# Optimization experiments

Measured on AMD Instinct MI355X. Metric: run time of the kernel, lower is better.

## Reference

```python
import jax, jax.numpy as jnp
import numpy as np

N_QUBITS = 12
DEPTH = 6
BATCH = 4096

# Wire 0 is the most-significant bit (PennyLane default.qubit convention).

def _rx(t):
    c = jnp.cos(t / 2).astype(jnp.complex64)
    s = (-1j * jnp.sin(t / 2)).astype(jnp.complex64)
    return jnp.stack([jnp.stack([c, s], -1), jnp.stack([s, c], -1)], -2)

def _ry(t):
    c = jnp.cos(t / 2).astype(jnp.complex64)
    s = jnp.sin(t / 2).astype(jnp.complex64)
    return jnp.stack([jnp.stack([c, -s], -1), jnp.stack([s, c], -1)], -2)

def _rz(t):
    em = jnp.exp(-1j * t.astype(jnp.complex64) / 2)
    ep = jnp.exp(1j * t.astype(jnp.complex64) / 2)
    z = jnp.zeros_like(em)
    return jnp.stack([jnp.stack([em, z], -1), jnp.stack([z, ep], -1)], -2)

def _apply_1q(state, gate, q, n):
    # state: (B, 2^n); gate: (2,2) shared or (B,2,2) batched
    B = state.shape[0]
    st = state.reshape(B, 1 << q, 2, 1 << (n - 1 - q))
    eq = 'ab,xlbr->xlar' if gate.ndim == 2 else 'xab,xlbr->xlar'
    return jnp.einsum(eq, gate, st).reshape(B, -1)

def _apply_cnot(state, c, n):
    # CNOT with control c, target c+1 (adjacent wires)
    B = state.shape[0]
    st = state.reshape(B, 1 << c, 2, 2, 1 << (n - 2 - c))
    st = jnp.concatenate([st[:, :, 0:1], st[:, :, 1:2, ::-1]], axis=2)
    return st.reshape(B, -1)

def _z_signs(n):
    idx = jnp.arange(1 << n)
    bits = (idx[None, :] >> (n - 1 - jnp.arange(n))[:, None]) & 1  # (n, 2^n)
    return (1.0 - 2.0 * bits).astype(jnp.float32)

def setup_inputs() -> dict:
    key = jax.random.key(0)
    k1, k2 = jax.random.split(key)
    x = jax.random.normal(k1, (BATCH, N_QUBITS), dtype=jnp.float32)
    params = jax.random.normal(k2, (DEPTH, N_QUBITS, 3), dtype=jnp.float32)
    return {"x": x, "params": params}

def reference(x, params):
    B, n = x.shape
    depth = params.shape[0]
    state = jnp.zeros((B, 1 << n), jnp.complex64).at[:, 0].set(1.0)
    # input encoding: batched RX per qubit
    for i in range(n):
        state = _apply_1q(state, _rx(x[:, i]), i, n)
    for d in range(depth):
        for i in range(n):
            state = _apply_1q(state, _ry(params[d, i, 0]), i, n)
            state = _apply_1q(state, _rz(params[d, i, 1]), i, n)
            state = _apply_1q(state, _rx(params[d, i, 2]), i, n)
        for i in range(n - 1):
            state = _apply_cnot(state, i, n)
    probs = state.real ** 2 + state.imag ** 2  # (B, 2^n)
    return probs @ _z_signs(n).T  # (B, n) Pauli-Z expvals
```

## Files before the change

### kernel.cpp

```cpp
#include <hip/hip_runtime.h>

#define NQ    12
#define DIM   4096
#define DEPTH 6
#define BLK   256
#define RJ    16


typedef float f32x2 __attribute__((ext_vector_type(2)));

__device__ __host__ __forceinline__ constexpr int sufxc(int v) {
  v ^= v >> 1; v ^= v >> 2; v ^= v >> 4; v ^= v >> 8; return v;
}
__device__ __host__ __forceinline__ constexpr int K1w(int j) { return (j << 4) ^ j; }
__device__ __host__ __forceinline__ constexpr int K2w(int j) { return j << 8; }
__device__ __host__ __forceinline__ constexpr int KCw(int j) {
  const int s4 = sufxc(j) & 15;
  const int p  = __builtin_popcount((unsigned)j) & 1;
  return (s4 << 8) | (p ? 0xF0 : 0);
}

__device__ __forceinline__ f32x2 pfma(f32x2 a, f32x2 b, f32x2 c) {
  return __builtin_elementwise_fma(a, b, c);
}

template <int B>
__device__ __forceinline__ void gate4(f32x2 (&amp)[RJ], float4 u0, float4 u1) {
  const f32x2 r00 = {u0.x, u0.x}, mi00 = {-u0.y, u0.y};
  const f32x2 r01 = {u0.z, u0.z}, mi01 = {-u0.w, u0.w};
  const f32x2 r10 = {u1.x, u1.x}, mi10 = {-u1.y, u1.y};
  const f32x2 r11 = {u1.z, u1.z}, mi11 = {-u1.w, u1.w};
#pragma unroll
  for (int m = 0; m < RJ / 2; ++m) {
    const int lo = m & ((1 << B) - 1);
    const int j0 = ((m >> B) << (B + 1)) | lo;
    const int j1 = j0 | (1 << B);
    const f32x2 a = amp[j0], b = amp[j1];
    const f32x2 ax = a.yx, bx = b.yx;
    f32x2 n0 = r00 * a;
    n0 = pfma(mi00, ax, n0);
    n0 = pfma(r01, b, n0);
    n0 = pfma(mi01, bx, n0);
    f32x2 n1 = r10 * a;
    n1 = pfma(mi10, ax, n1);
    n1 = pfma(r11, b, n1);
    n1 = pfma(mi11, bx, n1);
    amp[j0] = n0; amp[j1] = n1;
  }
}

__global__ void gate_prep(const float* __restrict__ params, float* __restrict__ gt) {
  const int T = threadIdx.x;
  if (T >= DEPTH * NQ) return;
  const float py = params[T * 3 + 0];
  const float pz = params[T * 3 + 1];
  const float px = params[T * 3 + 2];
  float sa, ca, sb, cb, sg, cg;
  __sincosf(py * 0.5f, &sa, &ca);
  __sincosf(pz * 0.5f, &sb, &cb);
  __sincosf(px * 0.5f, &sg, &cg);
  const float Ar = ca * cb, Ai = -ca * sb;
  const float Br = -sa * cb, Bi = sa * sb;
  const float Cr = sa * cb, Ci = sa * sb;
  const float Dr = ca * cb, Di = ca * sb;
  float* u = &gt[T * 8];
  u[0] = cg * Ar + sg * Ci;   u[1] = cg * Ai - sg * Cr;
  u[2] = cg * Br + sg * Di;   u[3] = cg * Bi - sg * Dr;
  u[4] = sg * Ai + cg * Cr;   u[5] = -sg * Ar + cg * Ci;
  u[6] = sg * Bi + cg * Dr;   u[7] = -sg * Br + cg * Di;
}

__global__ __launch_bounds__(BLK) void qsim_kernel(const float* __restrict__ x,
                                                   const float* __restrict__ gt,
                                                   float* __restrict__ out) {
  __shared__ f32x2 sm2[DIM];

  const int T = threadIdx.x;
  const int b = blockIdx.x;

  f32x2 amp[RJ];
  {
    float cs[NQ], sn[NQ];
#pragma unroll
    for (int i = 0; i < NQ; ++i) __sincosf(x[b * NQ + i] * 0.5f, &sn[i], &cs[i]);
    float hm = 1.0f;
#pragma unroll
    for (int i = 0; i < 8; ++i) hm *= ((T >> (7 - i)) & 1) ? sn[i] : cs[i];
    float mag[RJ];
    mag[0] = hm;
#pragma unroll
    for (int bb = 0; bb < 4; ++bb) {
#pragma unroll
      for (int j = 0; j < (1 << bb); ++j) {
        mag[j | (1 << bb)] = mag[j] * sn[11 - bb];
        mag[j] = mag[j] * cs[11 - bb];
      }
    }
    const int pt = __popc(T);
#pragma unroll
    for (int j = 0; j < RJ; ++j) {
      const float m = mag[j];
      const int k = (pt + __popc(j)) & 3;
      const float rr = (k & 1) ? 0.0f : ((k & 2) ? -m : m);
      const float ii = (k & 1) ? ((k & 2) ? m : -m) : 0.0f;
      amp[j] = (f32x2){rr, ii};
    }
  }

  const int A0w = (T << 4) ^ (T & 15);
  const int B0w = ((T >> 4) << 8) | (T & 15);
  const int C0w = T ^ ((T >> 4) & 15);
  const int CT  = sufxc(T) & 255;
  const int D0w = CT ^ ((CT >> 4) & 15);

#define SWEEP(D, WBASE)                                                       \
  {                                                                           \
    const float4* uv0 = (const float4*)&gt[((D) * NQ + (WBASE)) * 8];         \
    gate4<0>(amp, uv0[0], uv0[1]);                                            \
    const float4* uv1 = (const float4*)&gt[((D) * NQ + (WBASE) - 1) * 8];     \
    gate4<1>(amp, uv1[0], uv1[1]);                                            \
    const float4* uv2 = (const float4*)&gt[((D) * NQ + (WBASE) - 2) * 8];     \
    gate4<2>(amp, uv2[0], uv2[1]);                                            \
    const float4* uv3 = (const float4*)&gt[((D) * NQ + (WBASE) - 3) * 8];     \
    gate4<3>(amp, uv3[0], uv3[1]);                                            \
  }
#define ST_ALL(EXPR)                                                          \
  {                                                                           \
    _Pragma("unroll") for (int j = 0; j < RJ; ++j) { sm2[(EXPR)] = amp[j]; }  \
  }
#define LD_ALL(EXPR)                                                          \
  {                                                                           \
    _Pragma("unroll") for (int j = 0; j < RJ; ++j) { amp[j] = sm2[(EXPR)]; }  \
  }

#pragma unroll 1
  for (int d = 0; d < DEPTH; ++d) {
    SWEEP(d, 11)
    ST_ALL(A0w ^ j)
    LD_ALL(B0w ^ K1w(j))
    SWEEP(d, 7)
    ST_ALL(B0w ^ K1w(j))
    __syncthreads();
    LD_ALL(C0w ^ K2w(j))
    SWEEP(d, 3)
    __syncthreads();
    ST_ALL(D0w ^ KCw(j))
    __syncthreads();
    LD_ALL(A0w ^ j)
  }
#undef SWEEP
#undef ST_ALL
#undef LD_ALL

  float tot = 0.f, s0 = 0.f, s1 = 0.f, s2 = 0.f, s3 = 0.f;
#pragma unroll
  for (int j = 0; j < RJ; ++j) {
    const float p = fmaf(amp[j].x, amp[j].x, amp[j].y * amp[j].y);
    tot += p;
    s0 += (j & 1) ? -p : p;
    s1 += (j & 2) ? -p : p;
    s2 += (j & 4) ? -p : p;
    s3 += (j & 8) ? -p : p;
  }
  float v[NQ];
#pragma unroll
  for (int w = 0; w < 8; ++w) v[w] = ((T >> (7 - w)) & 1) ? -tot : tot;
  v[8] = s3; v[9] = s2; v[10] = s1; v[11] = s0;
#pragma unroll
  for (int w = 0; w < NQ; ++w) {
#pragma unroll
    for (int o = 32; o > 0; o >>= 1) v[w] += __shfl_xor(v[w], o);
  }
  __syncthreads();
  const int wv = T >> 6, lt = T & 63;
  float* smf = (float*)sm2;
  if (lt == 0) {
#pragma unroll
    for (int w = 0; w < NQ; ++w) smf[w * 4 + wv] = v[w];
  }
  __syncthreads();
  if (T < NQ) out[b * NQ + T] = (smf[T * 4 + 0] + smf[T * 4 + 1]) +
                                (smf[T * 4 + 2] + smf[T * 4 + 3]);
}

extern "C" void kernel_launch(void* const* d_in, const int* in_sizes, int n_in,
                              void* d_out, int out_size, void* d_ws, size_t ws_size,
                              hipStream_t stream) {
  const float* x      = (const float*)d_in[0];
  const float* params = (const float*)d_in[1];
  float* out          = (float*)d_out;
  float* gt           = (float*)d_ws;
  const int B = in_sizes[0] / NQ;
  gate_prep<<<1, 128, 0, stream>>>(params, gt);
  qsim_kernel<<<B, BLK, 0, stream>>>(x, gt, out);
}
```

Baseline: 238.2 us.

## Apply fused 4-qubit gate blocks via bf16 split-precision MFMA matrix multiplies

Replaces the per-thread scalar 2x2 gate sweeps with 16x16 complex unitaries, one per group of four wires, built by a prep kernel as Kronecker products. These are applied with bf16 MFMA instructions, using a hi/lo bf16 split of both the matrix and the state to keep near-fp32 accuracy. The state now lives in LDS as packed split-bf16 values with swizzled addressing, and the final probabilities are written to LDS for the reduction. The aim is to move the gate arithmetic onto the matrix cores, at the cost of extra pack/unpack work, more LDS traffic, more barriers, and some precision loss from the split representation.

```diff
diff --git a/kernel.cpp b/kernel.cpp
--- a/kernel.cpp
+++ b/kernel.cpp
@@ -4,81 +4,202 @@
 #define DIM   4096
 #define DEPTH 6
 #define BLK   256
-#define RJ    16
-
-
-typedef float f32x2 __attribute__((ext_vector_type(2)));
-
-__device__ __host__ __forceinline__ constexpr int sufxc(int v) {
-  v ^= v >> 1; v ^= v >> 2; v ^= v >> 4; v ^= v >> 8; return v;
-}
-__device__ __host__ __forceinline__ constexpr int K1w(int j) { return (j << 4) ^ j; }
-__device__ __host__ __forceinline__ constexpr int K2w(int j) { return j << 8; }
-__device__ __host__ __forceinline__ constexpr int KCw(int j) {
-  const int s4 = sufxc(j) & 15;
-  const int p  = __builtin_popcount((unsigned)j) & 1;
-  return (s4 << 8) | (p ? 0xF0 : 0);
-}
-
-__device__ __forceinline__ f32x2 pfma(f32x2 a, f32x2 b, f32x2 c) {
-  return __builtin_elementwise_fma(a, b, c);
-}
-
-template <int B>
-__device__ __forceinline__ void gate4(f32x2 (&amp)[RJ], float4 u0, float4 u1) {
-  const f32x2 r00 = {u0.x, u0.x}, mi00 = {-u0.y, u0.y};
-  const f32x2 r01 = {u0.z, u0.z}, mi01 = {-u0.w, u0.w};
-  const f32x2 r10 = {u1.x, u1.x}, mi10 = {-u1.y, u1.y};
-  const f32x2 r11 = {u1.z, u1.z}, mi11 = {-u1.w, u1.w};
-#pragma unroll
-  for (int m = 0; m < RJ / 2; ++m) {
-    const int lo = m & ((1 << B) - 1);
-    const int j0 = ((m >> B) << (B + 1)) | lo;
-    const int j1 = j0 | (1 << B);
-    const f32x2 a = amp[j0], b = amp[j1];
-    const f32x2 ax = a.yx, bx = b.yx;
-    f32x2 n0 = r00 * a;
-    n0 = pfma(mi00, ax, n0);
-    n0 = pfma(r01, b, n0);
-    n0 = pfma(mi01, bx, n0);
-    f32x2 n1 = r10 * a;
-    n1 = pfma(mi10, ax, n1);
-    n1 = pfma(r11, b, n1);
-    n1 = pfma(mi11, bx, n1);
-    amp[j0] = n0; amp[j1] = n1;
-  }
-}
-
-__global__ void gate_prep(const float* __restrict__ params, float* __restrict__ gt) {
-  const int T = threadIdx.x;
-  if (T >= DEPTH * NQ) return;
-  const float py = params[T * 3 + 0];
-  const float pz = params[T * 3 + 1];
-  const float px = params[T * 3 + 2];
-  float sa, ca, sb, cb, sg, cg;
-  __sincosf(py * 0.5f, &sa, &ca);
-  __sincosf(pz * 0.5f, &sb, &cb);
-  __sincosf(px * 0.5f, &sg, &cg);
-  const float Ar = ca * cb, Ai = -ca * sb;
-  const float Br = -sa * cb, Bi = sa * sb;
-  const float Cr = sa * cb, Ci = sa * sb;
-  const float Dr = ca * cb, Di = ca * sb;
-  float* u = &gt[T * 8];
-  u[0] = cg * Ar + sg * Ci;   u[1] = cg * Ai - sg * Cr;
-  u[2] = cg * Br + sg * Di;   u[3] = cg * Bi - sg * Dr;
-  u[4] = sg * Ai + cg * Cr;   u[5] = -sg * Ar + cg * Ci;
-  u[6] = sg * Bi + cg * Dr;   u[7] = -sg * Br + cg * Di;
+#define NT    4
+
+
+typedef __attribute__((ext_vector_type(8))) short bfrag;
+typedef __attribute__((ext_vector_type(4))) float f32x4v;
+typedef __attribute__((ext_vector_type(4))) int   i32x4v;
+typedef __attribute__((ext_vector_type(2))) unsigned u32x2v;
+
+__device__ __host__ __forceinline__ constexpr int sfx4(int v) {
+  v &= 15; v ^= v >> 1; v ^= v >> 2; return v & 15;
+}
+__device__ __host__ __forceinline__ constexpr int sfx8(int v) {
+  v &= 255; v ^= v >> 1; v ^= v >> 2; v ^= v >> 4; return v & 255;
+}
+__device__ __host__ __forceinline__ constexpr int par4(int v) {
+  return __builtin_popcount((unsigned)v) & 1;
+}
+__device__ __forceinline__ int pa(int c, int comp, int l) {
+  int uu = (comp << 2) | (l >> 2);
+  uu = (uu ^ (c & 7) ^ ((c >> 4) & 7)) & 7;
+  return (c << 7) + (uu << 4) + ((l & 3) << 2);
+}
+__device__ __host__ __forceinline__ constexpr int pa0(int cd, int ld) {
+  return (cd << 7) ^ (((((cd & 7) ^ ((cd >> 4) & 7)) ^ ((ld >> 2) & 3)) & 7) << 4)
+                   ^ ((ld & 3) << 2);
+}
+__device__ __host__ __forceinline__ constexpr int prodK(int P, int dd) {
+  return (P == 0) ? pa0(dd, 0)
+       : (P == 1) ? pa0(dd << 4, 0)
+       : pa0((sfx4(dd) << 4) | (par4(dd) * 15), par4(dd) * 15);
+}
+__device__ __host__ __forceinline__ constexpr int qK(int dd) {
+  return (sfx4(dd) << 8) | (par4(dd) * 255);
+}
+
+__device__ __forceinline__ unsigned rne16(unsigned u) {
+  return (u + 0x7FFFu + ((u >> 16) & 1u)) >> 16;
+}
+__device__ __forceinline__ unsigned packsplit(float x) {
+  const unsigned u = __float_as_uint(x);
+  const unsigned h = rne16(u);
+  const float hf = __uint_as_float(h << 16);
+  const unsigned l = rne16(__float_as_uint(x - hf));
+  return h | (l << 16);
+}
+
+__global__ void prep_kernel(const float* __restrict__ params, float* __restrict__ gt) {
+  const int s18 = blockIdx.x;
+  const int d = s18 / 3, p = s18 % 3;
+  const int L = threadIdx.x;
+  __shared__ float G[4][8];
+  if (L < 4) {
+    const int wire = 11 - 4 * p - L;
+    const float py = params[(d * NQ + wire) * 3 + 0];
+    const float pz = params[(d * NQ + wire) * 3 + 1];
+    const float px = params[(d * NQ + wire) * 3 + 2];
+    float sa, ca, sb, cb, sg, cg;
+    __sincosf(py * 0.5f, &sa, &ca);
+    __sincosf(pz * 0.5f, &sb, &cb);
+    __sincosf(px * 0.5f, &sg, &cg);
+    const float Ar = ca * cb, Ai = -ca * sb;
+    const float Br = -sa * cb, Bi = sa * sb;
+    const float Cr = sa * cb, Ci = sa * sb;
+    const float Dr = ca * cb, Di = ca * sb;
+    float* u = G[L];
+    u[0] = cg * Ar + sg * Ci;  u[1] = cg * Ai - sg * Cr;
+    u[2] = cg * Br + sg * Di;  u[3] = cg * Bi - sg * Dr;
+    u[4] = sg * Ai + cg * Cr;  u[5] = -sg * Ar + cg * Ci;
+    u[6] = sg * Bi + cg * Dr;  u[7] = -sg * Br + cg * Di;
+  }
+  __syncthreads();
+  const int r = L & 15, kg = L >> 4;
+  unsigned short frag[4][8];
+#pragma unroll
+  for (int e = 0; e < 8; ++e) {
+    const int kk = ((kg & 1) << 3) | e;
+    float cr = 1.f, ci = 0.f;
+#pragma unroll
+    for (int bb = 0; bb < 4; ++bb) {
+      const int cell = (((r >> bb) & 1) * 2 + ((kk >> bb) & 1)) * 2;
+      const float ar = G[bb][cell], ai = G[bb][cell + 1];
+      const float nr = cr * ar - ci * ai;
+      const float ni = cr * ai + ci * ar;
+      cr = nr; ci = ni;
+    }
+    const float vr = (kg >= 2) ? -ci : cr;
+    const float vi = (kg >= 2) ?  cr : ci;
+    const unsigned wr = packsplit(vr);
+    const unsigned wi = packsplit(vi);
+    frag[0][e] = (unsigned short)(wr & 0xFFFFu);
+    frag[1][e] = (unsigned short)(wr >> 16);
+    frag[2][e] = (unsigned short)(wi & 0xFFFFu);
+    frag[3][e] = (unsigned short)(wi >> 16);
+  }
+#pragma unroll
+  for (int mx = 0; mx < 4; ++mx) {
+    const unsigned q0 = (unsigned)frag[mx][0] | ((unsigned)frag[mx][1] << 16);
+    const unsigned q1 = (unsigned)frag[mx][2] | ((unsigned)frag[mx][3] << 16);
+    const unsigned q2 = (unsigned)frag[mx][4] | ((unsigned)frag[mx][5] << 16);
+    const unsigned q3 = (unsigned)frag[mx][6] | ((unsigned)frag[mx][7] << 16);
+    i32x4v vv = { (int)q0, (int)q1, (int)q2, (int)q3 };
+    *(i32x4v*)((char*)gt + (((s18 * 4 + mx) * 64) + L) * 16) = vv;
+  }
+}
+
+template <int P, bool FINAL>
+__device__ __forceinline__ void do_sweep(int d, const float* __restrict__ gt,
+                                         char* smb, int T) {
+  const int lane = T & 63, wv = T >> 6;
+  const int n = lane & 15, g = lane >> 4;
+  const int comp = lane >> 5, lhalf = g & 1;
+  const int s18 = d * 3 + P;
+
+  const i32x4v* gp = (const i32x4v*)gt + (s18 * 4) * 64 + lane;
+  const bfrag A0 = __builtin_bit_cast(bfrag, gp[0]);
+  const bfrag A1 = __builtin_bit_cast(bfrag, gp[64]);
+  const bfrag A2 = __builtin_bit_cast(bfrag, gp[128]);
+  const bfrag A3 = __builtin_bit_cast(bfrag, gp[192]);
+
+  i32x4v ra[NT], rb[NT];
+#pragma unroll
+  for (int t = 0; t < NT; ++t) {
+    const int TT = wv * NT + t;
+    const int a0 = pa(TT * 16 + n, comp, lhalf * 8);
+    ra[t] = *(const i32x4v*)(smb + a0);
+    rb[t] = *(const i32x4v*)(smb + (a0 ^ 16));
+  }
+  __syncthreads();
+
+#pragma unroll
+  for (int t = 0; t < NT; ++t) {
+    const int TT = wv * NT + t;
+    unsigned hh[4], ll[4];
+#pragma unroll
+    for (int i = 0; i < 2; ++i) {
+      const unsigned a = (unsigned)ra[t][2 * i], b2 = (unsigned)ra[t][2 * i + 1];
+      const unsigned c = (unsigned)rb[t][2 * i], d2 = (unsigned)rb[t][2 * i + 1];
+      hh[i]     = (a & 0xFFFFu) | (b2 << 16);
+      ll[i]     = (a >> 16)     | (b2 & 0xFFFF0000u);
+      hh[i + 2] = (c & 0xFFFFu) | (d2 << 16);
+      ll[i + 2] = (c >> 16)     | (d2 & 0xFFFF0000u);
+    }
+    i32x4v hv = { (int)hh[0], (int)hh[1], (int)hh[2], (int)hh[3] };
+    i32x4v lv = { (int)ll[0], (int)ll[1], (int)ll[2], (int)ll[3] };
+    const bfrag BH = __builtin_bit_cast(bfrag, hv);
+    const bfrag BL = __builtin_bit_cast(bfrag, lv);
+
+    f32x4v cr = { 0.f, 0.f, 0.f, 0.f }, ci = { 0.f, 0.f, 0.f, 0.f };
+    cr = __builtin_amdgcn_mfma_f32_16x16x32_bf16(A0, BH, cr, 0, 0, 0);
+    cr = __builtin_amdgcn_mfma_f32_16x16x32_bf16(A0, BL, cr, 0, 0, 0);
+    cr = __builtin_amdgcn_mfma_f32_16x16x32_bf16(A1, BH, cr, 0, 0, 0);
+    ci = __builtin_amdgcn_mfma_f32_16x16x32_bf16(A2, BH, ci, 0, 0, 0);
+    ci = __builtin_amdgcn_mfma_f32_16x16x32_bf16(A2, BL, ci, 0, 0, 0);
+    ci = __builtin_amdgcn_mfma_f32_16x16x32_bf16(A3, BH, ci, 0, 0, 0);
+
+    if (!FINAL) {
+      int base;
+      if (P == 0) {
+        base = pa((TT << 4) | (g << 2), 0, n);
+      } else if (P == 1) {
+        base = pa((g << 6) | n, 0, TT);
+      } else {
+        const int S8 = sfx8((TT << 4) | n);
+        const int PM = ((g ^ (g >> 1)) & 1) ? 15 : 0;
+        const int cb = (sfx4(g << 2) << 4) | (((S8 >> 4) ^ PM) & 15);
+        const int lb = (S8 ^ PM) & 15;
+        base = pa(cb, 0, lb);
+      }
+#pragma unroll
+      for (int dd = 0; dd < 4; ++dd) {
+        *(unsigned*)(smb + (base ^ prodK(P, dd)))        = packsplit(cr[dd]);
+        *(unsigned*)(smb + (base ^ prodK(P, dd) ^ 64))   = packsplit(ci[dd]);
+      }
+    } else {
+      const int S8 = sfx8((TT << 4) | n);
+      const int PM = ((g ^ (g >> 1)) & 1) ? 15 : 0;
+      const int cb = (sfx4(g << 2) << 4) | (((S8 >> 4) ^ PM) & 15);
+      const int lb = (S8 ^ PM) & 15;
+      const int qb = (cb << 4) | lb;
+#pragma unroll
+      for (int dd = 0; dd < 4; ++dd) {
+        const float pr = fmaf(cr[dd], cr[dd], ci[dd] * ci[dd]);
+        *(float*)(smb + ((qb ^ qK(dd)) << 2)) = pr;
+      }
+    }
+  }
+  __syncthreads();
 }
 
 __global__ __launch_bounds__(BLK) void qsim_kernel(const float* __restrict__ x,
                                                    const float* __restrict__ gt,
                                                    float* __restrict__ out) {
-  __shared__ f32x2 sm2[DIM];
-
-  const int T = threadIdx.x;
-  const int b = blockIdx.x;
-
-  f32x2 amp[RJ];
+  __shared__ __align__(16) unsigned smu[8192];
+  char* smb = (char*)smu;
+  const int T = threadIdx.x, b = blockIdx.x;
+
   {
     float cs[NQ], sn[NQ];
 #pragma unroll
@@ -86,76 +207,51 @@
     float hm = 1.0f;
 #pragma unroll
     for (int i = 0; i < 8; ++i) hm *= ((T >> (7 - i)) & 1) ? sn[i] : cs[i];
-    float mag[RJ];
+    float mag[16];
     mag[0] = hm;
 #pragma unroll
-    for (int bb = 0; bb < 4; ++bb) {
+    for (int bb = 0; bb < 4; ++bb)
 #pragma unroll
       for (int j = 0; j < (1 << bb); ++j) {
         mag[j | (1 << bb)] = mag[j] * sn[11 - bb];
-        mag[j] = mag[j] * cs[11 - bb];
-      }
-    }
+        mag[j]             = mag[j] * cs[11 - bb];
+      }
     const int pt = __popc(T);
-#pragma unroll
-    for (int j = 0; j < RJ; ++j) {
-      const float m = mag[j];
-      const int k = (pt + __popc(j)) & 3;
-      const float rr = (k & 1) ? 0.0f : ((k & 2) ? -m : m);
-      const float ii = (k & 1) ? ((k & 2) ? m : -m) : 0.0f;
-      amp[j] = (f32x2){rr, ii};
-    }
-  }
-
-  const int A0w = (T << 4) ^ (T & 15);
-  const int B0w = ((T >> 4) << 8) | (T & 15);
-  const int C0w = T ^ ((T >> 4) & 15);
-  const int CT  = sufxc(T) & 255;
-  const int D0w = CT ^ ((CT >> 4) & 15);
-
-#define SWEEP(D, WBASE)                                                       \
-  {                                                                           \
-    const float4* uv0 = (const float4*)&gt[((D) * NQ + (WBASE)) * 8];         \
-    gate4<0>(amp, uv0[0], uv0[1]);                                            \
-    const float4* uv1 = (const float4*)&gt[((D) * NQ + (WBASE) - 1) * 8];     \
-    gate4<1>(amp, uv1[0], uv1[1]);                                            \
-    const float4* uv2 = (const float4*)&gt[((D) * NQ + (WBASE) - 2) * 8];     \
-    gate4<2>(amp, uv2[0], uv2[1]);                                            \
-    const float4* uv3 = (const float4*)&gt[((D) * NQ + (WBASE) - 3) * 8];     \
-    gate4<3>(amp, uv3[0], uv3[1]);                                            \
-  }
-#define ST_ALL(EXPR)                                                          \
-  {                                                                           \
-    _Pragma("unroll") for (int j = 0; j < RJ; ++j) { sm2[(EXPR)] = amp[j]; }  \
-  }
-#define LD_ALL(EXPR)                                                          \
-  {                                                                           \
-    _Pragma("unroll") for (int j = 0; j < RJ; ++j) { amp[j] = sm2[(EXPR)]; }  \
-  }
+    float re[16], im[16];
+#pragma unroll
+    for (int l = 0; l < 16; ++l) {
+      const float m = mag[l];
+      const int k = (pt + __popc(l)) & 3;
+      re[l] = (k & 1) ? 0.f : ((k & 2) ? -m : m);
+      im[l] = (k & 1) ? ((k & 2) ? m : -m) : 0.f;
+    }
+#pragma unroll
+    for (int cc = 0; cc < 2; ++cc)
+#pragma unroll
+      for (int l = 0; l < 16; l += 2) {
+        u32x2v wv2;
+        wv2.x = packsplit(cc ? im[l]     : re[l]);
+        wv2.y = packsplit(cc ? im[l + 1] : re[l + 1]);
+        *(u32x2v*)(smb + pa(T, cc, l)) = wv2;
+      }
+  }
+  __syncthreads();
 
 #pragma unroll 1
-  for (int d = 0; d < DEPTH; ++d) {
-    SWEEP(d, 11)
-    ST_ALL(A0w ^ j)
-    LD_ALL(B0w ^ K1w(j))
-    SWEEP(d, 7)
-    ST_ALL(B0w ^ K1w(j))
-    __syncthreads();
-    LD_ALL(C0w ^ K2w(j))
-    SWEEP(d, 3)
-    __syncthreads();
-    ST_ALL(D0w ^ KCw(j))
-    __syncthreads();
-    LD_ALL(A0w ^ j)
-  }
-#undef SWEEP
-#undef ST_ALL
-#undef LD_ALL
-
+  for (int d = 0; d < DEPTH - 1; ++d) {
+    do_sweep<0, false>(d, gt, smb, T);
+    do_sweep<1, false>(d, gt, smb, T);
+    do_sweep<2, false>(d, gt, smb, T);
+  }
+  do_sweep<0, false>(DEPTH - 1, gt, smb, T);
+  do_sweep<1, false>(DEPTH - 1, gt, smb, T);
+  do_sweep<2, true >(DEPTH - 1, gt, smb, T);
+
+  const float* smf = (const float*)smu;
   float tot = 0.f, s0 = 0.f, s1 = 0.f, s2 = 0.f, s3 = 0.f;
 #pragma unroll
-  for (int j = 0; j < RJ; ++j) {
-    const float p = fmaf(amp[j].x, amp[j].x, amp[j].y * amp[j].y);
+  for (int j = 0; j < 16; ++j) {
+    const float p = smf[T * 16 + j];
     tot += p;
     s0 += (j & 1) ? -p : p;
     s1 += (j & 2) ? -p : p;
@@ -167,20 +263,16 @@
   for (int w = 0; w < 8; ++w) v[w] = ((T >> (7 - w)) & 1) ? -tot : tot;
   v[8] = s3; v[9] = s2; v[10] = s1; v[11] = s0;
 #pragma unroll
-  for (int w = 0; w < NQ; ++w) {
+  for (int w = 0; w < NQ; ++w)
 #pragma unroll
     for (int o = 32; o > 0; o >>= 1) v[w] += __shfl_xor(v[w], o);
-  }
-  __syncthreads();
-  const int wv = T >> 6, lt = T & 63;
-  float* smf = (float*)sm2;
-  if (lt == 0) {
-#pragma unroll
-    for (int w = 0; w < NQ; ++w) smf[w * 4 + wv] = v[w];
-  }
-  __syncthreads();
-  if (T < NQ) out[b * NQ + T] = (smf[T * 4 + 0] + smf[T * 4 + 1]) +
-                                (smf[T * 4 + 2] + smf[T * 4 + 3]);
+  float* scr = (float*)(smb + 16384);
+  if ((T & 63) == 0)
+#pragma unroll
+    for (int w = 0; w < NQ; ++w) scr[w * 4 + (T >> 6)] = v[w];
+  __syncthreads();
+  if (T < NQ) out[b * NQ + T] = (scr[T * 4 + 0] + scr[T * 4 + 1]) +
+                                (scr[T * 4 + 2] + scr[T * 4 + 3]);
 }
 
 extern "C" void kernel_launch(void* const* d_in, const int* in_sizes, int n_in,
@@ -191,6 +283,6 @@
   float* out          = (float*)d_out;
   float* gt           = (float*)d_ws;
   const int B = in_sizes[0] / NQ;
-  gate_prep<<<1, 128, 0, stream>>>(params, gt);
+  prep_kernel<<<18, 64, 0, stream>>>(params, gt);
   qsim_kernel<<<B, BLK, 0, stream>>>(x, gt, out);
 }
```

Result: slower. 273.6 us (+14.8%).
